# Performance work log

Measured on AMD Instinct MI355X. Metric: run time of the kernel, lower is better.

The kernel has to match this reference:

```python
import math
import jax, jax.numpy as jnp
import numpy as np

EMB = 1024
HEADS = 16
HEAD_DIM = EMB // HEADS


def setup_inputs() -> dict:
    key = jax.random.key(0)
    ks = jax.random.split(key, 6)
    b, l = 4, 4096
    x = jax.random.normal(ks[0], (b, l, EMB), dtype=jnp.float32)
    # torch Linear weight shape (out, in); xavier_normal std = sqrt(2/(in+out))
    std = math.sqrt(2.0 / (EMB + EMB))
    Wq = jax.random.normal(ks[1], (EMB, EMB), dtype=jnp.float32) * std
    Wk = jax.random.normal(ks[2], (EMB, EMB), dtype=jnp.float32) * std
    Wv = jax.random.normal(ks[3], (EMB, EMB), dtype=jnp.float32) * std
    Wu = jax.random.normal(ks[4], (EMB, EMB), dtype=jnp.float32) * std
    Wo = jax.random.normal(ks[5], (EMB, EMB), dtype=jnp.float32) * std
    return {"x": x, "Wq": Wq, "Wk": Wk, "Wv": Wv, "Wu": Wu, "Wo": Wo}


def _srms_norm(x, eps=1e-12):
    # SRMSNorm over last dim with scale 1/sqrt(head_dims), computed in fp32
    dtype = x.dtype
    xf = x.astype(jnp.float32)
    scale = 1.0 / math.sqrt(x.shape[-1])
    n = jnp.linalg.norm(xf * scale, axis=-1, keepdims=True)
    return (xf / jnp.maximum(n, eps)).astype(dtype)


def reference(x, Wq, Wk, Wv, Wu, Wo):
    b, l, d = x.shape
    h, hd = HEADS, HEAD_DIM
    scale = math.sqrt(hd)

    def proj(W):
        return jnp.einsum('bld,ed->ble', x, W).reshape(b, l, h, hd).transpose(0, 2, 1, 3)

    q = jax.nn.relu(proj(Wq)) / scale        # (b,h,l,hd)
    k = jax.nn.relu(proj(Wk)) / scale
    v = proj(Wv)
    u = jax.nn.silu(proj(Wu))

    kv = jnp.einsum('bhlk,bhlv->bhkv', k, v)  # (b,h,hd,hd) state
    out = jnp.einsum('bhlk,bhkv->bhlv', q, kv)
    out = _srms_norm(out) * u
    out = out.transpose(0, 2, 1, 3).reshape(b, l, d)
    return jnp.einsum('bld,ed->ble', out, Wo)
```

## Files before the change

### kernel.cpp

```cpp
#include <hip/hip_runtime.h>

typedef _Float16 f16;
typedef _Float16 f16x4 __attribute__((ext_vector_type(4)));
typedef _Float16 f16x8 __attribute__((ext_vector_type(8)));
typedef float f32x4 __attribute__((ext_vector_type(4)));

#define EMB 1024
#define SEQL 4096
#define BATCH 4
#define NH 16
#define HD 64
#define BH 64
#define MROWS 16384
#define KVSPLIT 16

#define GLOAD_LDS(gp, lp) \
    __builtin_amdgcn_global_load_lds((const __attribute__((address_space(1))) void*)(gp), \
                                     (__attribute__((address_space(3))) void*)(lp), 16, 0, 0)

struct WPtrs { const float* p[5]; };

#define NXB (MROWS * EMB / 4 / 256)
#define NWB (5 * EMB * EMB / 4 / 256)
#define NZB (BH * HD * HD / 4 / 256)
__global__ void prep_kernel(const float* __restrict__ x, WPtrs wp,
                            f16* __restrict__ x16, f16* __restrict__ w16,
                            float4* __restrict__ kvz)
{
    int gid = blockIdx.x;
    int t = threadIdx.x;
    if (gid < NXB) {
        int i = gid * 256 + t;
        float4 v = ((const float4*)x)[i];
        f16x4 o = { (f16)v.x, (f16)v.y, (f16)v.z, (f16)v.w };
        ((f16x4*)x16)[i] = o;
    } else if (gid < NXB + NWB) {
        int i = (gid - NXB) * 256 + t;
        int wsel = i >> 18;
        int j = i & 262143;
        float4 v = ((const float4*)wp.p[wsel])[j];
        f16x4 o = { (f16)v.x, (f16)v.y, (f16)v.z, (f16)v.w };
        ((f16x4*)(w16 + (size_t)wsel * EMB * EMB))[j] = o;
    } else {
        int i = (gid - NXB - NWB) * 256 + t;
        kvz[i] = float4{0.f, 0.f, 0.f, 0.f};
    }
}


#define FENCE asm volatile("" ::: "memory")
#define WAITV(N) asm volatile("s_waitcnt vmcnt(" #N ")" ::: "memory")
#define BAR do { FENCE; __builtin_amdgcn_s_barrier(); FENCE; } while (0)

template<int MODE>
__global__ __launch_bounds__(512, 2) void gemm_kernel(
    const f16* __restrict__ A, const f16* __restrict__ Bt,
    void* __restrict__ Cv, int M, int N, int K)
{
    __shared__ f16 As[2][256 * 64];
    __shared__ f16 Bs[2][256 * 64];

    const int tid  = threadIdx.x;
    const int lane = tid & 63;
    const int w    = tid >> 6;
    const int rw   = lane & 15;
    const int quad = lane >> 4;
    const int wm   = w >> 2;
    const int wn   = w & 3;

    const f16* Ap = A;
    const f16* Bp = Bt;
    char* Cp = (char*)Cv;
    bool sel_qu = true;
    int m0, n0;
    if (MODE == 34) {
        int bid = blockIdx.x;
        if (bid < 512) {
            m0 = (bid >> 3) * 256; n0 = (bid & 7) * 256;
        } else {
            bid -= 512;
            m0 = (bid >> 6) * 256; n0 = (bid & 63) * 256;
            Ap = Bt + (size_t)2 * EMB * EMB;
            Bp = A;
            Cp = (char*)Cv + (size_t)2 * MROWS * EMB * 2;
            sel_qu = false;
        }
    } else {
        m0 = blockIdx.y * 256; n0 = blockIdx.x * 256;
    }
    const size_t Ks = (size_t)K;
    const int NT = K >> 6;

    const int srow8 = lane >> 3;
    const int slog  = (lane & 7) ^ srow8;
    const f16* gA = Ap + (size_t)(m0 + w * 8 + srow8) * Ks + slog * 8;
    const f16* gB = Bp + (size_t)(n0 + w * 8 + srow8) * Ks + slog * 8;
    const int lst = w * 512;

#define STAGE_A(H, T, BUF) do { \
    GLOAD_LDS(gA + (size_t)((H) * 128 +  0) * Ks + (T) * 64, &As[BUF][(H) * 8192 + lst]); \
    GLOAD_LDS(gA + (size_t)((H) * 128 + 64) * Ks + (T) * 64, &As[BUF][(H) * 8192 + 4096 + lst]); \
} while (0)
#define STAGE_B(H, T, BUF) do { \
    GLOAD_LDS(gB + (size_t)((H) * 128 +  0) * Ks + (T) * 64, &Bs[BUF][(H) * 8192 + lst]); \
    GLOAD_LDS(gB + (size_t)((H) * 128 + 64) * Ks + (T) * 64, &Bs[BUF][(H) * 8192 + 4096 + lst]); \
} while (0)

    const int rw7   = rw & 7;
    const int s0o   = ( quad      ^ rw7) * 8;
    const int s1o   = ((quad + 4) ^ rw7) * 8;
    const int abase = (wm * 64 + rw) * 64;
    const int bbase = (wn * 32 + rw) * 64;

    f32x4 acc[2][2][4][2] = {};
    f16x8 af[4][2], bf[2][2];

#define READ_A(QM, BUF) do { \
    _Pragma("unroll") \
    for (int mi = 0; mi < 4; ++mi) { \
        af[mi][0] = *(const f16x8*)&As[BUF][(QM) * 8192 + abase + mi * 1024 + s0o]; \
        af[mi][1] = *(const f16x8*)&As[BUF][(QM) * 8192 + abase + mi * 1024 + s1o]; \
    } \
} while (0)
#define READ_B(QN, BUF) do { \
    _Pragma("unroll") \
    for (int nj = 0; nj < 2; ++nj) { \
        bf[nj][0] = *(const f16x8*)&Bs[BUF][(QN) * 8192 + bbase + nj * 1024 + s0o]; \
        bf[nj][1] = *(const f16x8*)&Bs[BUF][(QN) * 8192 + bbase + nj * 1024 + s1o]; \
    } \
} while (0)
#define MFMA_Q(QM, QN) do { \
    __builtin_amdgcn_s_setprio(1); \
    _Pragma("unroll") \
    for (int mi = 0; mi < 4; ++mi) \
        _Pragma("unroll") \
        for (int nj = 0; nj < 2; ++nj) { \
            acc[QM][QN][mi][nj] = __builtin_amdgcn_mfma_f32_16x16x32_f16(bf[nj][0], af[mi][0], acc[QM][QN][mi][nj], 0, 0, 0); \
            acc[QM][QN][mi][nj] = __builtin_amdgcn_mfma_f32_16x16x32_f16(bf[nj][1], af[mi][1], acc[QM][QN][mi][nj], 0, 0, 0); \
        } \
    __builtin_amdgcn_s_setprio(0); \
} while (0)

    STAGE_A(0, 0, 0);
    STAGE_B(0, 0, 0);
    STAGE_B(1, 0, 0);
    STAGE_A(1, 0, 0);
    if (NT > 1) { STAGE_A(0, 1, 1); WAITV(2); } else { WAITV(0); }
    BAR;

    for (int kt = 0; kt < NT; ++kt) {
        const int cur = kt & 1, nxt = cur ^ 1;
        const bool p1 = (kt + 1 < NT), p2 = (kt + 2 < NT);
        READ_A(0, cur); READ_B(0, cur);
        if (p1) STAGE_B(0, kt + 1, nxt);
        BAR; MFMA_Q(0, 0); BAR;
        READ_B(1, cur);
        if (p1) { STAGE_B(1, kt + 1, nxt); WAITV(6); } else { WAITV(0); }
        BAR; MFMA_Q(0, 1); BAR;
        READ_A(1, cur);
        if (p1) STAGE_A(1, kt + 1, nxt);
        BAR; MFMA_Q(1, 1); BAR;
        READ_B(0, cur);
        if (p2) { STAGE_A(0, kt + 2, cur); WAITV(4); }
        else if (p1) { WAITV(2); }
        BAR; MFMA_Q(1, 0); BAR;
    }

    #pragma unroll
    for (int qm = 0; qm < 2; ++qm)
    #pragma unroll
    for (int qn = 0; qn < 2; ++qn)
    #pragma unroll
    for (int mi = 0; mi < 4; ++mi)
    #pragma unroll
    for (int nj = 0; nj < 2; ++nj) {
        const int m_idx = m0 + qm * 128 + wm * 64 + mi * 16 + rw;
        const int n_idx = n0 + qn * 128 + wn * 32 + nj * 16 + quad * 4;
        f32x4 a = acc[qm][qn][mi][nj];
        if (MODE == 0) {
            float4 vv = { a[0], a[1], a[2], a[3] };
            *(float4*)&((float*)Cv)[(size_t)m_idx * N + n_idx] = vv;
        } else if (sel_qu) {
            int sel = n_idx >> 10, e = n_idx & 1023;
            int b = m_idx >> 12, l = m_idx & 4095, h = e >> 6, hdi = e & 63;
            f16x4 o;
            #pragma unroll
            for (int r = 0; r < 4; r++) {
                float v = a[r];
                o[r] = (f16)(sel ? (v / (1.0f + __expf(-v))) : (fmaxf(v, 0.0f) * 0.125f));
            }
            *(f16x4*)&((f16*)Cp)[(size_t)sel * MROWS * EMB +
                                 (((size_t)(b * 16 + h) * 4096 + l) << 6) + hdi] = o;
        } else {
            int sel = m_idx >> 10, e = m_idx & 1023;
            int b = n_idx >> 12, l = n_idx & 4095;
            f16x4 o;
            #pragma unroll
            for (int r = 0; r < 4; r++) {
                float v = a[r];
                o[r] = (f16)(sel ? v : (fmaxf(v, 0.0f) * 0.125f));
            }
            *(f16x4*)&((f16*)Cp)[(size_t)sel * MROWS * EMB +
                                 (((size_t)b * 1024 + e) << 12) + l] = o;
        }
    }
#undef STAGE_A
#undef STAGE_B
#undef READ_A
#undef READ_B
#undef MFMA_Q
}

__global__ __launch_bounds__(256) void kv_split_kernel(
    const f16* __restrict__ kT, const f16* __restrict__ vT, float* __restrict__ kv32)
{
    const int bh    = blockIdx.x;
    const int chunk = blockIdx.y;
    const int lane  = threadIdx.x & 63;
    const int w     = threadIdx.x >> 6;
    const int rw    = lane & 15;
    const int quad  = lane >> 4;
    const int lbase = chunk * (SEQL / KVSPLIT);

    const f16* kp = kT + (size_t)bh * HD * SEQL + (size_t)(w * 16 + rw) * SEQL + lbase + quad * 8;
    const f16* vp = vT + (size_t)bh * HD * SEQL + (size_t)rw * SEQL + lbase + quad * 8;

    f32x4 acc[4] = {};
    for (int k0 = 0; k0 < SEQL / KVSPLIT; k0 += 32) {
        f16x8 a = *(const f16x8*)(kp + k0);
        #pragma unroll
        for (int t = 0; t < 4; t++) {
            f16x8 b = *(const f16x8*)(vp + (size_t)16 * t * SEQL + k0);
            acc[t] = __builtin_amdgcn_mfma_f32_16x16x32_f16(a, b, acc[t], 0, 0, 0);
        }
    }
    float* out = kv32 + (size_t)bh * HD * HD;
    #pragma unroll
    for (int t = 0; t < 4; t++)
        #pragma unroll
        for (int r = 0; r < 4; r++)
            atomicAdd(&out[(w * 16 + quad * 4 + r) * 64 + t * 16 + rw], acc[t][r]);
}

__global__ __launch_bounds__(256) void ret_out_kernel(
    const f16* __restrict__ q, const f16* __restrict__ u,
    const float* __restrict__ kv32, f16* __restrict__ o)
{
    const int bh    = blockIdx.x;
    const int chunk = blockIdx.y;
    const int lane  = threadIdx.x & 63;
    const int w     = threadIdx.x >> 6;
    const int rw    = lane & 15;
    const int quad  = lane >> 4;

    const float* kvp = kv32 + (size_t)bh * 4096;
    f16x8 bf[2][4];
    #pragma unroll
    for (int s = 0; s < 2; s++)
        #pragma unroll
        for (int t = 0; t < 4; t++)
            #pragma unroll
            for (int j = 0; j < 8; j++)
                bf[s][t][j] = (f16)kvp[(s * 32 + quad * 8 + j) * 64 + t * 16 + rw];

    const f16* qp = q + (size_t)bh * SEQL * HD;
    const f16* up = u + (size_t)bh * SEQL * HD;
    const int b = bh >> 4, h = bh & 15;
    f16* op = o + (size_t)b * SEQL * EMB + h * 64;

    const int l_wave = chunk * 512 + w * 128;
    for (int s = 0; s < 8; s++) {
        const int l0 = l_wave + s * 16;
        f16x8 a0 = *(const f16x8*)(qp + (size_t)(l0 + rw) * 64 + quad * 8);
        f16x8 a1 = *(const f16x8*)(qp + (size_t)(l0 + rw) * 64 + 32 + quad * 8);
        f32x4 acc[4] = {};
        #pragma unroll
        for (int t = 0; t < 4; t++) {
            acc[t] = __builtin_amdgcn_mfma_f32_16x16x32_f16(a0, bf[0][t], acc[t], 0, 0, 0);
            acc[t] = __builtin_amdgcn_mfma_f32_16x16x32_f16(a1, bf[1][t], acc[t], 0, 0, 0);
        }
        float inv[4];
        #pragma unroll
        for (int r = 0; r < 4; r++) {
            float ss = acc[0][r] * acc[0][r] + acc[1][r] * acc[1][r]
                     + acc[2][r] * acc[2][r] + acc[3][r] * acc[3][r];
            #pragma unroll
            for (int msk = 1; msk < 16; msk <<= 1)
                ss += __shfl_xor(ss, msk, 16);
            inv[r] = 8.0f / fmaxf(sqrtf(ss), 8e-12f);
        }
        #pragma unroll
        for (int t = 0; t < 4; t++)
            #pragma unroll
            for (int r = 0; r < 4; r++) {
                int l = l0 + quad * 4 + r;
                int col = t * 16 + rw;
                float uval = (float)up[(size_t)l * 64 + col];
                op[(size_t)l * EMB + col] = (f16)(acc[t][r] * inv[r] * uval);
            }
    }
}

extern "C" void kernel_launch(void* const* d_in, const int* in_sizes, int n_in,
                              void* d_out, int out_size, void* d_ws, size_t ws_size,
                              hipStream_t stream)
{
    const float* x = (const float*)d_in[0];
    WPtrs wp;
    wp.p[0] = (const float*)d_in[1];
    wp.p[1] = (const float*)d_in[4];
    wp.p[2] = (const float*)d_in[2];
    wp.p[3] = (const float*)d_in[3];
    wp.p[4] = (const float*)d_in[5];

    char* ws = (char*)d_ws;
    size_t off = 0;
    f16* x16 = (f16*)(ws + off); off += (size_t)MROWS * EMB * 2;
    f16* w16 = (f16*)(ws + off); off += (size_t)5 * EMB * EMB * 2;
    f16* qb  = (f16*)(ws + off); off += (size_t)MROWS * EMB * 2;
    f16* ub  = (f16*)(ws + off); off += (size_t)MROWS * EMB * 2;
    f16* kTb = (f16*)(ws + off); off += (size_t)MROWS * EMB * 2;
    f16* vTb = (f16*)(ws + off); off += (size_t)MROWS * EMB * 2;
    float* kv32 = (float*)(ws + off); off += (size_t)BH * HD * HD * 4;
    f16* ob  = x16;
    (void)ub; (void)vTb;

    prep_kernel<<<NXB + NWB + NZB, 256, 0, stream>>>(x, wp, x16, w16, (float4*)kv32);

    f16* Wo = w16 + (size_t)4 * EMB * EMB;

    gemm_kernel<34><<<1024, 512, 0, stream>>>(x16, w16, qb, MROWS, 2 * EMB, EMB);

    kv_split_kernel<<<dim3(BH, KVSPLIT), dim3(256), 0, stream>>>(kTb, vTb, kv32);
    ret_out_kernel<<<dim3(BH, 8), dim3(256), 0, stream>>>(qb, ub, kv32, ob);

    gemm_kernel<0><<<dim3(4, 64), dim3(512), 0, stream>>>(ob, Wo, d_out, MROWS, EMB, EMB);
}
```

Before: 376.0 us.

## Transpose MFMA output so each lane owns a row; vectorize norm epilogue; reduce KV split

Swaps the MFMA operand order so the accumulator holds a row per lane, which turns the per-row norm reduction from 4 cross-lane 16-wide shuffle trees into a local sum plus two shuffles. The u loads and output stores become 4-wide f16 vectors instead of scalar scattered accesses. Separately, KVSPLIT drops from 16 to 4, which changes how the kv-state reduction is partitioned and trades fewer partial sums for less parallelism in that stage.

```diff
diff --git a/kernel.cpp b/kernel.cpp
--- a/kernel.cpp
+++ b/kernel.cpp
@@ -12,7 +12,7 @@
 #define HD 64
 #define BH 64
 #define MROWS 16384
-#define KVSPLIT 16
+#define KVSPLIT 4
 
 #define GLOAD_LDS(gp, lp) \
     __builtin_amdgcn_global_load_lds((const __attribute__((address_space(1))) void*)(gp), \
@@ -276,28 +276,28 @@
         f32x4 acc[4] = {};
         #pragma unroll
         for (int t = 0; t < 4; t++) {
-            acc[t] = __builtin_amdgcn_mfma_f32_16x16x32_f16(a0, bf[0][t], acc[t], 0, 0, 0);
-            acc[t] = __builtin_amdgcn_mfma_f32_16x16x32_f16(a1, bf[1][t], acc[t], 0, 0, 0);
-        }
-        float inv[4];
-        #pragma unroll
-        for (int r = 0; r < 4; r++) {
-            float ss = acc[0][r] * acc[0][r] + acc[1][r] * acc[1][r]
-                     + acc[2][r] * acc[2][r] + acc[3][r] * acc[3][r];
-            #pragma unroll
-            for (int msk = 1; msk < 16; msk <<= 1)
-                ss += __shfl_xor(ss, msk, 16);
-            inv[r] = 8.0f / fmaxf(sqrtf(ss), 8e-12f);
-        }
+            acc[t] = __builtin_amdgcn_mfma_f32_16x16x32_f16(bf[0][t], a0, acc[t], 0, 0, 0);
+            acc[t] = __builtin_amdgcn_mfma_f32_16x16x32_f16(bf[1][t], a1, acc[t], 0, 0, 0);
+        }
+        float ss = 0.f;
         #pragma unroll
         for (int t = 0; t < 4; t++)
             #pragma unroll
-            for (int r = 0; r < 4; r++) {
-                int l = l0 + quad * 4 + r;
-                int col = t * 16 + rw;
-                float uval = (float)up[(size_t)l * 64 + col];
-                op[(size_t)l * EMB + col] = (f16)(acc[t][r] * inv[r] * uval);
-            }
+            for (int r = 0; r < 4; r++)
+                ss += acc[t][r] * acc[t][r];
+        ss += __shfl_xor(ss, 16);
+        ss += __shfl_xor(ss, 32);
+        const float inv = 8.0f / fmaxf(sqrtf(ss), 8e-12f);
+        #pragma unroll
+        for (int t = 0; t < 4; t++) {
+            const int col = t * 16 + quad * 4;
+            f16x4 uv = *(const f16x4*)(up + (size_t)(l0 + rw) * 64 + col);
+            f16x4 o4;
+            #pragma unroll
+            for (int r = 0; r < 4; r++)
+                o4[r] = (f16)(acc[t][r] * inv * (float)uv[r]);
+            *(f16x4*)&op[(size_t)(l0 + rw) * EMB + col] = o4;
+        }
     }
 }
 
```

New measurement: 374.3 us, median of 2. No clear change (-0.5%).
